# Kernel optimization log

Measured on AMD Instinct MI355X. Metric: run time of the kernel, lower is better.

Reference implementation:

```python
import jax, jax.numpy as jnp
import numpy as np

ALPHA = 1.0  # softness coefficient


def _soft_assign(data, centroids):
    # data: (B, N, D), centroids: (B, K, D)
    # squared euclidean distance -> (B, N, K)
    dist = jnp.sum((data[:, :, None, :] - centroids[:, None, :, :]) ** 2, axis=-1)
    return jax.nn.softmax(-ALPHA * dist, axis=2)


def _update_once(data, probs):
    # weighted centroid update: (B, K, D)
    denom = jnp.sum(probs, axis=1)  # (B, K)
    centroids = jnp.einsum('bnk,bnd->bkd', probs, data) / denom[:, :, None]
    probs = _soft_assign(data, centroids)
    return probs, centroids


def setup_inputs() -> dict:
    key = jax.random.key(0)
    k1, k2 = jax.random.split(key)
    B, N, D, K = 8, 65536, 40, 2
    data = jax.random.normal(k1, (B, N, D), dtype=jnp.float32)
    centroid_ids = jax.random.randint(k2, (B, K), 0, N)
    return {"data": data, "centroid_ids": centroid_ids, "iteration": 10}


def reference(data, centroid_ids, iteration):
    # init centroids by gathering selected samples (random init path)
    centroids = jnp.take_along_axis(data, centroid_ids[:, :, None], axis=1)  # (B, K, D)
    probs = _soft_assign(data, centroids)

    def body(i, carry):
        probs, _ = carry
        return _update_once(data, probs)

    probs, centroids = jax.lax.fori_loop(0, iteration, body, (probs, centroids))
    return probs
```

## Files before the change

### kernel.cpp

```cpp
#include <hip/hip_runtime.h>
#include <hip/hip_fp16.h>
#include <cstddef>

#define BB    8
#define NN    65536
#define DD    40
#define NITER 10

#define PREPB  128
#define PTPB   256
#define PTILES 2
#define PSTR   21
#define ROW1   84
#define PBLK   64
#define TPB    256
#define PPT    4
#define ROW    44


__device__ __forceinline__ float rfl(float x) {
    return __int_as_float(__builtin_amdgcn_readfirstlane(__float_as_int(x)));
}
__device__ __forceinline__ float prob0(float diff) {
    return __builtin_amdgcn_rcpf(1.f + __expf(diff));
}
__device__ __forceinline__ float2 h2f(unsigned u) {
    return __half22float2(*(const __half2*)&u);
}

__device__ __forceinline__ void gh_from_ids(const float* __restrict__ data,
                                            const int* __restrict__ ids, int b,
                                            float gs[DD], float& hs, int tid) {
    __shared__ float gbuf[DD], sqbuf[DD], hbuf;
    if (tid < DD) {
        const int i0 = ids[b * 2 + 0];
        const int i1 = ids[b * 2 + 1];
        const float c0 = data[((size_t)b * NN + i0) * DD + tid];
        const float c1 = data[((size_t)b * NN + i1) * DD + tid];
        gbuf[tid]  = c0 - c1;
        sqbuf[tid] = c0 * c0 - c1 * c1;
    }
    __syncthreads();
    if (tid == 0) {
        float h = 0.f;
#pragma unroll
        for (int i = 0; i < DD; ++i) h += sqbuf[i];
        hbuf = h;
    }
    __syncthreads();
#pragma unroll
    for (int i = 0; i < DD; ++i) gs[i] = rfl(gbuf[i]);
    hs = rfl(hbuf);
    __syncthreads();
}

__device__ __forceinline__ void gh_first(const float* __restrict__ pp,
                                         float* __restrict__ Sg, int b,
                                         float gs[DD], float& hs, int tid) {
    __shared__ float part[81][2];
    __shared__ float red[81], gbuf[DD], sqbuf[DD], hbuf;
    if (tid < 162) {
        const int v = tid % 81, q = tid / 81;
        const float* base = pp + (size_t)b * PREPB * ROW1;
        float s = 0.f;
#pragma unroll 8
        for (int j = 0; j < 64; ++j)
            s += base[(size_t)(q * 64 + j) * ROW1 + v];
        part[v][q] = s;
    }
    __syncthreads();
    if (tid < 81) red[tid] = part[tid][0] + part[tid][1];
    __syncthreads();
    if (tid < DD) {
        const float num = red[tid], den = red[DD];
        const float Sd  = red[41 + tid];
        Sg[b * DD + tid] = Sd;
        const float c0 = num / den;
        const float c1 = (Sd - num) / ((float)NN - den);
        gbuf[tid]  = c0 - c1;
        sqbuf[tid] = c0 * c0 - c1 * c1;
    }
    __syncthreads();
    if (tid == 0) {
        float h = 0.f;
#pragma unroll
        for (int i = 0; i < DD; ++i) h += sqbuf[i];
        hbuf = h;
    }
    __syncthreads();
#pragma unroll
    for (int i = 0; i < DD; ++i) gs[i] = rfl(gbuf[i]);
    hs = rfl(hbuf);
    __syncthreads();
}

__device__ __forceinline__ void gh_iter(const float* __restrict__ pp,
                                        const float* __restrict__ S, int b,
                                        float gs[DD], float& hs, int tid) {
    __shared__ float part[41][4];
    __shared__ float red[41], gbuf[DD], sqbuf[DD], hbuf;
    if (tid < 164) {
        const int v = tid % 41, q = tid / 41;
        const float* base = pp + (size_t)b * PBLK * ROW;
        float s = 0.f;
#pragma unroll 8
        for (int j = 0; j < 16; ++j)
            s += base[(size_t)(q * 16 + j) * ROW + v];
        part[v][q] = s;
    }
    __syncthreads();
    if (tid < 41)
        red[tid] = (part[tid][0] + part[tid][1]) + (part[tid][2] + part[tid][3]);
    __syncthreads();
    if (tid < DD) {
        const float num = red[tid], den = red[DD];
        const float c0 = num / den;
        const float c1 = (S[b * DD + tid] - num) / ((float)NN - den);
        gbuf[tid]  = c0 - c1;
        sqbuf[tid] = c0 * c0 - c1 * c1;
    }
    __syncthreads();
    if (tid == 0) {
        float h = 0.f;
#pragma unroll
        for (int i = 0; i < DD; ++i) h += sqbuf[i];
        hbuf = h;
    }
    __syncthreads();
#pragma unroll
    for (int i = 0; i < DD; ++i) gs[i] = rfl(gbuf[i]);
    hs = rfl(hbuf);
    __syncthreads();
}


__global__ __launch_bounds__(PTPB, 3) void k_prep(const float* __restrict__ data,
                                                  const int* __restrict__ ids,
                                                  __half2* __restrict__ dataT,
                                                  float* __restrict__ ppOut) {
    const int bid = blockIdx.x;
    const int b = bid & 7, pb = bid >> 3;
    const int tid = threadIdx.x;
    __shared__ unsigned stg[PTPB * PSTR];
    __half2* stgh = (__half2*)stg;

    float gs[DD], hs;
    gh_from_ids(data, ids, b, gs, hs, tid);

    float vals[2 * DD + 1];
#pragma unroll
    for (int i = 0; i <= 2 * DD; ++i) vals[i] = 0.f;

#pragma unroll
    for (int t = 0; t < PTILES; ++t) {
        const int basePt = pb * (PTPB * PTILES) + t * PTPB;
        const float4* src = (const float4*)(data + ((size_t)b * NN + basePt) * DD);
        __syncthreads();
#pragma unroll
        for (int j = 0; j < 10; ++j) {
            const unsigned f = tid + j * PTPB;
            const float4 v = src[f];
            const unsigned slot = (f / 10u) * PSTR + (f % 10u) * 2u;
            stgh[slot]     = __floats2half2_rn(v.x, v.y);
            stgh[slot + 1] = __floats2half2_rn(v.z, v.w);
        }
        __syncthreads();
        __half2 xh[20];
        const __half2* rp = stgh + tid * PSTR;
#pragma unroll
        for (int q = 0; q < 20; ++q) xh[q] = rp[q];

        __half2* dst = dataT + (size_t)b * (DD / 2) * NN + basePt + tid;
#pragma unroll
        for (int q = 0; q < 20; ++q) dst[(size_t)q * NN] = xh[q];

        float a0 = 0.f, a1 = 0.f, a2 = 0.f, a3 = 0.f;
#pragma unroll
        for (int q = 0; q < 20; ++q) {
            const float2 v = __half22float2(xh[q]);
            vals[41 + 2 * q] += v.x; vals[41 + 2 * q + 1] += v.y;
            if (q & 1) { a2 = fmaf(v.x, gs[2 * q], a2); a3 = fmaf(v.y, gs[2 * q + 1], a3); }
            else       { a0 = fmaf(v.x, gs[2 * q], a0); a1 = fmaf(v.y, gs[2 * q + 1], a1); }
        }
        const float p0 = prob0(fmaf(-2.f, (a0 + a1) + (a2 + a3), hs));
        vals[DD] += p0;
#pragma unroll
        for (int q = 0; q < 20; ++q) {
            const float2 v = __half22float2(xh[q]);
            vals[2 * q]     = fmaf(p0, v.x, vals[2 * q]);
            vals[2 * q + 1] = fmaf(p0, v.y, vals[2 * q + 1]);
        }
    }

#pragma unroll
    for (int i = 0; i <= 2 * DD; ++i) {
        vals[i] += __shfl_xor(vals[i], 32, 64);
        vals[i] += __shfl_xor(vals[i], 16, 64);
    }
    float* rbuf = (float*)stg;
    __shared__ float part2[2 * DD + 1][2];
    __syncthreads();
    const int lane = tid & 63, wave = tid >> 6;
    if (lane < 16) {
        const int row = wave * 16 + lane;
#pragma unroll
        for (int i = 0; i <= 2 * DD; ++i) rbuf[row * 84 + i] = vals[i];
    }
    __syncthreads();
    if (tid < 162) {
        const int v = tid % 81, q = tid / 81;
        float s = 0.f;
#pragma unroll 8
        for (int j = 0; j < 32; ++j) s += rbuf[(q * 32 + j) * 84 + v];
        part2[v][q] = s;
    }
    __syncthreads();
    if (tid < 81)
        ppOut[(size_t)(b * PREPB + pb) * ROW1 + tid] = part2[tid][0] + part2[tid][1];
}

template <int MODE, int FIRST>
__global__ __launch_bounds__(TPB, 2) void k_pass(const __half2* __restrict__ dataT,
                                                 const float* __restrict__ ppIn,
                                                 float* __restrict__ Sg,
                                                 float* __restrict__ ppOut,
                                                 float* __restrict__ out) {
    const int bid = blockIdx.x;
    const int b = bid & 7, pb = bid >> 3;
    const int tid = threadIdx.x;

    const int n0 = pb * (TPB * PPT) + tid * PPT;
    const __half2* basep = dataT + (size_t)b * (DD / 2) * NN + n0;
    unsigned xh0[20], xh1[20], xh2[20], xh3[20];
#pragma unroll
    for (int dp = 0; dp < DD / 2; ++dp) {
        const uint4 u = *(const uint4*)(basep + (size_t)dp * NN);
        xh0[dp] = u.x; xh1[dp] = u.y; xh2[dp] = u.z; xh3[dp] = u.w;
    }

    float gs[DD], hs;
    if constexpr (FIRST) gh_first(ppIn, Sg, b, gs, hs, tid);
    else                 gh_iter(ppIn, Sg, b, gs, hs, tid);

    float a00 = 0.f, a01 = 0.f, a10 = 0.f, a11 = 0.f;
    float a20 = 0.f, a21 = 0.f, a30 = 0.f, a31 = 0.f;
#pragma unroll
    for (int dp = 0; dp < DD / 2; ++dp) {
        const float2 v0 = h2f(xh0[dp]), v1 = h2f(xh1[dp]);
        const float2 v2 = h2f(xh2[dp]), v3 = h2f(xh3[dp]);
        a00 = fmaf(v0.x, gs[2 * dp], a00); a01 = fmaf(v0.y, gs[2 * dp + 1], a01);
        a10 = fmaf(v1.x, gs[2 * dp], a10); a11 = fmaf(v1.y, gs[2 * dp + 1], a11);
        a20 = fmaf(v2.x, gs[2 * dp], a20); a21 = fmaf(v2.y, gs[2 * dp + 1], a21);
        a30 = fmaf(v3.x, gs[2 * dp], a30); a31 = fmaf(v3.y, gs[2 * dp + 1], a31);
    }
    const float p00 = prob0(fmaf(-2.f, a00 + a01, hs));
    const float p01 = prob0(fmaf(-2.f, a10 + a11, hs));
    const float p02 = prob0(fmaf(-2.f, a20 + a21, hs));
    const float p03 = prob0(fmaf(-2.f, a30 + a31, hs));

    if constexpr (MODE == 2) {
        float4* o = (float4*)(out + ((size_t)b * NN + n0) * 2);
        o[0] = make_float4(p00, 1.f - p00, p01, 1.f - p01);
        o[1] = make_float4(p02, 1.f - p02, p03, 1.f - p03);
    } else {
        float acc[DD + 1];
#pragma unroll
        for (int i = 0; i < DD; ++i) acc[i] = 0.f;
        acc[DD] = (p00 + p01) + (p02 + p03);
#pragma unroll
        for (int dp = 0; dp < DD / 2; ++dp) {
            const float2 v0 = h2f(xh0[dp]), v1 = h2f(xh1[dp]);
            const float2 v2 = h2f(xh2[dp]), v3 = h2f(xh3[dp]);
            acc[2 * dp]     = fmaf(p00, v0.x, fmaf(p01, v1.x,
                              fmaf(p02, v2.x, fmaf(p03, v3.x, acc[2 * dp]))));
            acc[2 * dp + 1] = fmaf(p00, v0.y, fmaf(p01, v1.y,
                              fmaf(p02, v2.y, fmaf(p03, v3.y, acc[2 * dp + 1]))));
        }

#pragma unroll
        for (int i = 0; i <= DD; ++i) {
            acc[i] += __shfl_xor(acc[i], 32, 64);
            acc[i] += __shfl_xor(acc[i], 16, 64);
        }
        __shared__ float rbuf[64 * ROW];
        __shared__ float part2[DD + 1][4];
        const int lane = tid & 63, wave = tid >> 6;
        if (lane < 16) {
            const int row = wave * 16 + lane;
#pragma unroll
            for (int i = 0; i <= DD; ++i) rbuf[row * ROW + i] = acc[i];
        }
        __syncthreads();
        if (tid < 164) {
            const int v = tid % 41, q = tid / 41;
            float s = 0.f;
#pragma unroll
            for (int j = 0; j < 16; ++j) s += rbuf[(q * 16 + j) * ROW + v];
            part2[v][q] = s;
        }
        __syncthreads();
        if (tid <= DD)
            ppOut[(size_t)(b * PBLK + pb) * ROW + tid] =
                (part2[tid][0] + part2[tid][1]) + (part2[tid][2] + part2[tid][3]);
    }
}


extern "C" void kernel_launch(void* const* d_in, const int* in_sizes, int n_in,
                              void* d_out, int out_size, void* d_ws, size_t ws_size,
                              hipStream_t stream) {
    const float* data = (const float*)d_in[0];
    const int*   ids  = (const int*)d_in[1];

    float* ws      = (float*)d_ws;
    __half2* dataT = (__half2*)ws;
    float* pA      = ws + (size_t)BB * (DD / 2) * NN;
    float* pp1     = pA + (size_t)BB * PREPB * ROW1;
    float* pp2     = pp1 + (size_t)BB * PBLK * ROW;
    float* Sg      = pp2 + (size_t)BB * PBLK * ROW;
    float* out     = (float*)d_out;

    k_prep<<<PREPB * BB, PTPB, 0, stream>>>(data, ids, dataT, pA);

    const int grid = PBLK * BB;
    k_pass<1, 1><<<grid, TPB, 0, stream>>>(dataT, pA, Sg, pp1, nullptr);
    const float* cur = pp1;
    float* nxt = pp2;
    for (int t = 0; t < NITER - 2; ++t) {
        k_pass<1, 0><<<grid, TPB, 0, stream>>>(dataT, cur, Sg, nxt, nullptr);
        const float* tmp = cur; cur = nxt; nxt = (float*)tmp;
    }
    k_pass<2, 0><<<grid, TPB, 0, stream>>>(dataT, cur, Sg, nullptr, out);
}
```

Before: 137.1 us.

## Split prep into pure transpose kernel plus separate first-pass kernel

The fused prep kernel, which transposed data to fp16 and also computed the initial soft assignment and partial sums, is split in two. A lean transpose kernel with higher occupancy runs first, then a new k_pass1 kernel reads the transposed fp16 data and computes the first probabilities, weighted sums and the per-dimension sums. This aims to cut the register pressure and low occupancy of the fused kernel. The cost is an extra launch and a second read of the transposed data.

```diff
diff --git a/kernel.cpp b/kernel.cpp
--- a/kernel.cpp
+++ b/kernel.cpp
@@ -31,26 +31,26 @@
 __device__ __forceinline__ void gh_from_ids(const float* __restrict__ data,
                                             const int* __restrict__ ids, int b,
                                             float gs[DD], float& hs, int tid) {
-    __shared__ float gbuf[DD], sqbuf[DD], hbuf;
+    __shared__ float gbuf0[DD], sqbuf0[DD], hbuf0;
     if (tid < DD) {
         const int i0 = ids[b * 2 + 0];
         const int i1 = ids[b * 2 + 1];
         const float c0 = data[((size_t)b * NN + i0) * DD + tid];
         const float c1 = data[((size_t)b * NN + i1) * DD + tid];
-        gbuf[tid]  = c0 - c1;
-        sqbuf[tid] = c0 * c0 - c1 * c1;
+        gbuf0[tid]  = c0 - c1;
+        sqbuf0[tid] = c0 * c0 - c1 * c1;
     }
     __syncthreads();
     if (tid == 0) {
         float h = 0.f;
 #pragma unroll
-        for (int i = 0; i < DD; ++i) h += sqbuf[i];
-        hbuf = h;
-    }
-    __syncthreads();
-#pragma unroll
-    for (int i = 0; i < DD; ++i) gs[i] = rfl(gbuf[i]);
-    hs = rfl(hbuf);
+        for (int i = 0; i < DD; ++i) h += sqbuf0[i];
+        hbuf0 = h;
+    }
+    __syncthreads();
+#pragma unroll
+    for (int i = 0; i < DD; ++i) gs[i] = rfl(gbuf0[i]);
+    hs = rfl(hbuf0);
     __syncthreads();
 }
 
@@ -61,11 +61,11 @@
     __shared__ float red[81], gbuf[DD], sqbuf[DD], hbuf;
     if (tid < 162) {
         const int v = tid % 81, q = tid / 81;
-        const float* base = pp + (size_t)b * PREPB * ROW1;
+        const float* base = pp + (size_t)b * PBLK * ROW1;
         float s = 0.f;
 #pragma unroll 8
-        for (int j = 0; j < 64; ++j)
-            s += base[(size_t)(q * 64 + j) * ROW1 + v];
+        for (int j = 0; j < 32; ++j)
+            s += base[(size_t)(q * 32 + j) * ROW1 + v];
         part[v][q] = s;
     }
     __syncthreads();
@@ -134,28 +134,19 @@
 }
 
 
-__global__ __launch_bounds__(PTPB, 3) void k_prep(const float* __restrict__ data,
-                                                  const int* __restrict__ ids,
-                                                  __half2* __restrict__ dataT,
-                                                  float* __restrict__ ppOut) {
+__global__ __launch_bounds__(PTPB, 6) void k_trans(const float* __restrict__ data,
+                                                   __half2* __restrict__ dataT) {
     const int bid = blockIdx.x;
     const int b = bid & 7, pb = bid >> 3;
     const int tid = threadIdx.x;
     __shared__ unsigned stg[PTPB * PSTR];
     __half2* stgh = (__half2*)stg;
 
-    float gs[DD], hs;
-    gh_from_ids(data, ids, b, gs, hs, tid);
-
-    float vals[2 * DD + 1];
-#pragma unroll
-    for (int i = 0; i <= 2 * DD; ++i) vals[i] = 0.f;
-
 #pragma unroll
     for (int t = 0; t < PTILES; ++t) {
         const int basePt = pb * (PTPB * PTILES) + t * PTPB;
         const float4* src = (const float4*)(data + ((size_t)b * NN + basePt) * DD);
-        __syncthreads();
+        if (t) __syncthreads();
 #pragma unroll
         for (int j = 0; j < 10; ++j) {
             const unsigned f = tid + j * PTPB;
@@ -165,58 +156,89 @@
             stgh[slot + 1] = __floats2half2_rn(v.z, v.w);
         }
         __syncthreads();
-        __half2 xh[20];
+        __half2* dst = dataT + (size_t)b * (DD / 2) * NN + basePt + tid;
         const __half2* rp = stgh + tid * PSTR;
 #pragma unroll
-        for (int q = 0; q < 20; ++q) xh[q] = rp[q];
-
-        __half2* dst = dataT + (size_t)b * (DD / 2) * NN + basePt + tid;
-#pragma unroll
-        for (int q = 0; q < 20; ++q) dst[(size_t)q * NN] = xh[q];
-
-        float a0 = 0.f, a1 = 0.f, a2 = 0.f, a3 = 0.f;
-#pragma unroll
-        for (int q = 0; q < 20; ++q) {
-            const float2 v = __half22float2(xh[q]);
-            vals[41 + 2 * q] += v.x; vals[41 + 2 * q + 1] += v.y;
-            if (q & 1) { a2 = fmaf(v.x, gs[2 * q], a2); a3 = fmaf(v.y, gs[2 * q + 1], a3); }
-            else       { a0 = fmaf(v.x, gs[2 * q], a0); a1 = fmaf(v.y, gs[2 * q + 1], a1); }
-        }
-        const float p0 = prob0(fmaf(-2.f, (a0 + a1) + (a2 + a3), hs));
-        vals[DD] += p0;
-#pragma unroll
-        for (int q = 0; q < 20; ++q) {
-            const float2 v = __half22float2(xh[q]);
-            vals[2 * q]     = fmaf(p0, v.x, vals[2 * q]);
-            vals[2 * q + 1] = fmaf(p0, v.y, vals[2 * q + 1]);
-        }
+        for (int q = 0; q < 20; ++q) dst[(size_t)q * NN] = rp[q];
+    }
+}
+
+__global__ __launch_bounds__(TPB, 2) void k_pass1(const __half2* __restrict__ dataT,
+                                                  const float* __restrict__ data,
+                                                  const int* __restrict__ ids,
+                                                  float* __restrict__ ppOut) {
+    const int bid = blockIdx.x;
+    const int b = bid & 7, pb = bid >> 3;
+    const int tid = threadIdx.x;
+
+    const int n0 = pb * (TPB * PPT) + tid * PPT;
+    const __half2* basep = dataT + (size_t)b * (DD / 2) * NN + n0;
+    unsigned xh0[20], xh1[20], xh2[20], xh3[20];
+#pragma unroll
+    for (int dp = 0; dp < DD / 2; ++dp) {
+        const uint4 u = *(const uint4*)(basep + (size_t)dp * NN);
+        xh0[dp] = u.x; xh1[dp] = u.y; xh2[dp] = u.z; xh3[dp] = u.w;
+    }
+
+    float gs[DD], hs;
+    gh_from_ids(data, ids, b, gs, hs, tid);
+
+    float a00 = 0.f, a01 = 0.f, a10 = 0.f, a11 = 0.f;
+    float a20 = 0.f, a21 = 0.f, a30 = 0.f, a31 = 0.f;
+#pragma unroll
+    for (int dp = 0; dp < DD / 2; ++dp) {
+        const float2 v0 = h2f(xh0[dp]), v1 = h2f(xh1[dp]);
+        const float2 v2 = h2f(xh2[dp]), v3 = h2f(xh3[dp]);
+        a00 = fmaf(v0.x, gs[2 * dp], a00); a01 = fmaf(v0.y, gs[2 * dp + 1], a01);
+        a10 = fmaf(v1.x, gs[2 * dp], a10); a11 = fmaf(v1.y, gs[2 * dp + 1], a11);
+        a20 = fmaf(v2.x, gs[2 * dp], a20); a21 = fmaf(v2.y, gs[2 * dp + 1], a21);
+        a30 = fmaf(v3.x, gs[2 * dp], a30); a31 = fmaf(v3.y, gs[2 * dp + 1], a31);
+    }
+    const float p00 = prob0(fmaf(-2.f, a00 + a01, hs));
+    const float p01 = prob0(fmaf(-2.f, a10 + a11, hs));
+    const float p02 = prob0(fmaf(-2.f, a20 + a21, hs));
+    const float p03 = prob0(fmaf(-2.f, a30 + a31, hs));
+
+    float acc[2 * DD + 1];
+#pragma unroll
+    for (int i = 0; i < DD; ++i) acc[i] = 0.f;
+    acc[DD] = (p00 + p01) + (p02 + p03);
+#pragma unroll
+    for (int dp = 0; dp < DD / 2; ++dp) {
+        const float2 v0 = h2f(xh0[dp]), v1 = h2f(xh1[dp]);
+        const float2 v2 = h2f(xh2[dp]), v3 = h2f(xh3[dp]);
+        acc[2 * dp]     = fmaf(p00, v0.x, fmaf(p01, v1.x,
+                          fmaf(p02, v2.x, fmaf(p03, v3.x, acc[2 * dp]))));
+        acc[2 * dp + 1] = fmaf(p00, v0.y, fmaf(p01, v1.y,
+                          fmaf(p02, v2.y, fmaf(p03, v3.y, acc[2 * dp + 1]))));
+        acc[41 + 2 * dp]     = (v0.x + v1.x) + (v2.x + v3.x);
+        acc[41 + 2 * dp + 1] = (v0.y + v1.y) + (v2.y + v3.y);
     }
 
 #pragma unroll
     for (int i = 0; i <= 2 * DD; ++i) {
-        vals[i] += __shfl_xor(vals[i], 32, 64);
-        vals[i] += __shfl_xor(vals[i], 16, 64);
-    }
-    float* rbuf = (float*)stg;
-    __shared__ float part2[2 * DD + 1][2];
-    __syncthreads();
+        acc[i] += __shfl_xor(acc[i], 32, 64);
+        acc[i] += __shfl_xor(acc[i], 16, 64);
+    }
+    __shared__ float rbuf[64 * ROW1];
+    __shared__ float part2[81][2];
     const int lane = tid & 63, wave = tid >> 6;
     if (lane < 16) {
         const int row = wave * 16 + lane;
 #pragma unroll
-        for (int i = 0; i <= 2 * DD; ++i) rbuf[row * 84 + i] = vals[i];
+        for (int i = 0; i <= 2 * DD; ++i) rbuf[row * ROW1 + i] = acc[i];
     }
     __syncthreads();
     if (tid < 162) {
         const int v = tid % 81, q = tid / 81;
         float s = 0.f;
 #pragma unroll 8
-        for (int j = 0; j < 32; ++j) s += rbuf[(q * 32 + j) * 84 + v];
+        for (int j = 0; j < 32; ++j) s += rbuf[(q * 32 + j) * ROW1 + v];
         part2[v][q] = s;
     }
     __syncthreads();
     if (tid < 81)
-        ppOut[(size_t)(b * PREPB + pb) * ROW1 + tid] = part2[tid][0] + part2[tid][1];
+        ppOut[(size_t)(b * PBLK + pb) * ROW1 + tid] = part2[tid][0] + part2[tid][1];
 }
 
 template <int MODE, int FIRST>
@@ -283,7 +305,7 @@
             acc[i] += __shfl_xor(acc[i], 16, 64);
         }
         __shared__ float rbuf[64 * ROW];
-        __shared__ float part2[DD + 1][4];
+        __shared__ float part2[41][4];
         const int lane = tid & 63, wave = tid >> 6;
         if (lane < 16) {
             const int row = wave * 16 + lane;
@@ -315,14 +337,15 @@
     float* ws      = (float*)d_ws;
     __half2* dataT = (__half2*)ws;
     float* pA      = ws + (size_t)BB * (DD / 2) * NN;
-    float* pp1     = pA + (size_t)BB * PREPB * ROW1;
+    float* pp1     = pA + (size_t)BB * PBLK * ROW1;
     float* pp2     = pp1 + (size_t)BB * PBLK * ROW;
     float* Sg      = pp2 + (size_t)BB * PBLK * ROW;
     float* out     = (float*)d_out;
 
-    k_prep<<<PREPB * BB, PTPB, 0, stream>>>(data, ids, dataT, pA);
+    k_trans<<<PREPB * BB, PTPB, 0, stream>>>(data, dataT);
 
     const int grid = PBLK * BB;
+    k_pass1<<<grid, TPB, 0, stream>>>(dataT, data, ids, pA);
     k_pass<1, 1><<<grid, TPB, 0, stream>>>(dataT, pA, Sg, pp1, nullptr);
     const float* cur = pp1;
     float* nxt = pp2;
```

Measured after the change: 142.2 us. 3.7% more time.
